# Optimization experiments

Measured on AMD Instinct MI355X. Metric: run time of the kernel, lower is better.

Reference implementation:

```python
import jax, jax.numpy as jnp
import numpy as np


def setup_inputs() -> dict:
    key = jax.random.key(0)
    ks = jax.random.split(key, 4)
    T, B, E = 2048, 2, 1024
    query = jax.random.normal(ks[0], (T, B, E), dtype=jnp.float32)
    attn_mask = jnp.zeros((T, T), dtype=jnp.float32)
    Wqkv = jax.random.normal(ks[1], (3 * E, E), dtype=jnp.float32) * 0.02
    bqkv = jnp.zeros((3 * E,), dtype=jnp.float32)
    Wout = jax.random.normal(ks[2], (E, E), dtype=jnp.float32) * 0.02
    bout = jnp.zeros((E,), dtype=jnp.float32)
    return {"query": query, "attn_mask": attn_mask, "Wqkv": Wqkv,
            "bqkv": bqkv, "Wout": Wout, "bout": bout, "num_heads": 16}


def reference(query, attn_mask, Wqkv, bqkv, Wout, bout, num_heads):
    T, B, E = query.shape
    H = num_heads
    hd = E // H
    scaling = hd ** -0.5
    # fused QKV projection: [T,B,3E]
    qkv = jnp.einsum('tbe,fe->tbf', query, Wqkv) + bqkv
    q, k, v = jnp.split(qkv, 3, axis=-1)
    q = q * scaling
    # [T,B,E] -> [B*H, T, hd]
    def to_heads(x):
        return x.reshape(T, B * H, hd).transpose(1, 0, 2)
    q, k, v = to_heads(q), to_heads(k), to_heads(v)
    # scores [B*H, T, T]
    scores = jnp.einsum('bth,bsh->bts', q, k) + attn_mask[None, :, :]
    probs = jax.nn.softmax(scores, axis=-1)  # dropout p=0
    attn = jnp.einsum('bts,bsh->bth', probs, v)  # [B*H, T, hd]
    attn = attn.transpose(1, 0, 2).reshape(T, B, E)
    out = jnp.einsum('tbe,fe->tbf', attn, Wout) + bout
    avg_w = probs.reshape(B, H, T, T).sum(axis=1) / H
    return out, avg_w
```

## Files before the change

kernel.cpp:

```cpp
#include <hip/hip_runtime.h>
#include <cstdint>
#include <cstddef>

#define Tt 2048
#define Bb 2
#define Ee 1024
#define Hh 16
#define HD 64
#define BHh (Bb*Hh)
#define Mm (Tt*Bb)

typedef short bf16x8 __attribute__((ext_vector_type(8)));
typedef float f32x4  __attribute__((ext_vector_type(4)));

#define MFMA16(a,b,c) __builtin_amdgcn_mfma_f32_16x16x32_bf16(a, b, c, 0, 0, 0)

__device__ __forceinline__ unsigned short f2bf(float f) {
    unsigned int u = __builtin_bit_cast(unsigned int, f);
    u += 0x7FFFu + ((u >> 16) & 1u);
    return (unsigned short)(u >> 16);
}
__device__ __forceinline__ unsigned int pack2bf(float lo, float hi) {
    return (unsigned int)f2bf(lo) | ((unsigned int)f2bf(hi) << 16);
}

__device__ __forceinline__ int swzA(int row, int dwcol) {
    return (row*32 + dwcol) ^ ((row & 7) << 2);
}
__device__ __forceinline__ int swzG(int row, int dwcol) {
    return (row*16 + dwcol) ^ ((row & 3) << 2);
}

__device__ __forceinline__ bf16x8 ldfrag(const unsigned short* base, int row, int col) {
    const unsigned int* p = (const unsigned int*)(base + row*66 + col);
    const unsigned int* q = (const unsigned int*)(base + row*66 + col + 16);
    uint4 u;
    u.x = p[0]; u.y = p[1];
    u.z = q[0]; u.w = q[1];
    return __builtin_bit_cast(bf16x8, u);
}

__global__ __launch_bounds__(256)
void to_bf16(const float* __restrict__ src, unsigned short* __restrict__ dst, int n8)
{
    const int stride = gridDim.x * 256;
    for (int i = blockIdx.x*256 + threadIdx.x; i < n8; i += stride) {
        const float4 a = ((const float4*)src)[2*i];
        const float4 b = ((const float4*)src)[2*i + 1];
        const uint4 u = {pack2bf(a.x,a.y), pack2bf(a.z,a.w),
                         pack2bf(b.x,b.y), pack2bf(b.z,b.w)};
        ((uint4*)dst)[i] = u;
    }
}

template<int MODE>
__global__ __launch_bounds__(256)
void gemm_mfma(const unsigned short* __restrict__ A, const unsigned short* __restrict__ W,
               const float* __restrict__ bias, float* __restrict__ Cout,
               unsigned short* __restrict__ qbuf, unsigned short* __restrict__ kbuf,
               unsigned short* __restrict__ vbuf, int N, int K)
{
    __shared__ __align__(16) unsigned int AsDW[2][128*16];
    __shared__ __align__(16) unsigned int WsDW[2][128*16];
    const int tid  = threadIdx.x;
    const int bm   = blockIdx.y * 128;
    const int bn   = blockIdx.x * 128;
    const int w    = tid >> 6;
    const int lane = tid & 63;
    const int lr   = lane & 15;
    const int lg   = lane >> 4;
    const int wm   = (w >> 1) * 64;
    const int wn   = (w & 1) * 64;

    f32x4 acc[4][4];
#pragma unroll
    for (int m = 0; m < 4; ++m)
#pragma unroll
        for (int n = 0; n < 4; ++n)
            acc[m][n] = f32x4{0.f, 0.f, 0.f, 0.f};

    const int r1  = tid >> 2;
    const int cdw = (tid & 3) * 4;

    {
        const uint4 a0 = *(const uint4*)&A[(size_t)(bm + r1)      * K + cdw*2];
        const uint4 a1 = *(const uint4*)&A[(size_t)(bm + r1 + 64) * K + cdw*2];
        const uint4 w0 = *(const uint4*)&W[(size_t)(bn + r1)      * K + cdw*2];
        const uint4 w1 = *(const uint4*)&W[(size_t)(bn + r1 + 64) * K + cdw*2];
        *(uint4*)(AsDW[0] + swzG(r1,      cdw)) = a0;
        *(uint4*)(AsDW[0] + swzG(r1 + 64, cdw)) = a1;
        *(uint4*)(WsDW[0] + swzG(r1,      cdw)) = w0;
        *(uint4*)(WsDW[0] + swzG(r1 + 64, cdw)) = w1;
        __syncthreads();
    }

    int cur = 0;
    for (int k0 = 0; k0 < K; k0 += 32) {
        const bool has_next = (k0 + 32 < K);
        uint4 an0, an1, wn0, wn1;
        if (has_next) {
            an0 = *(const uint4*)&A[(size_t)(bm + r1)      * K + k0 + 32 + cdw*2];
            an1 = *(const uint4*)&A[(size_t)(bm + r1 + 64) * K + k0 + 32 + cdw*2];
            wn0 = *(const uint4*)&W[(size_t)(bn + r1)      * K + k0 + 32 + cdw*2];
            wn1 = *(const uint4*)&W[(size_t)(bn + r1 + 64) * K + k0 + 32 + cdw*2];
        }

        const unsigned int* Ac = AsDW[cur];
        const unsigned int* Wc = WsDW[cur];
        bf16x8 af[4], wf[4];
#pragma unroll
        for (int i = 0; i < 4; ++i) {
            af[i] = __builtin_bit_cast(bf16x8, *(const uint4*)(Ac + swzG(wm + 16*i + lr, 4*lg)));
            wf[i] = __builtin_bit_cast(bf16x8, *(const uint4*)(Wc + swzG(wn + 16*i + lr, 4*lg)));
        }
#pragma unroll
        for (int m = 0; m < 4; ++m)
#pragma unroll
            for (int n = 0; n < 4; ++n)
                acc[m][n] = MFMA16(af[m], wf[n], acc[m][n]);

        if (has_next) {
            *(uint4*)(AsDW[cur ^ 1] + swzG(r1,      cdw)) = an0;
            *(uint4*)(AsDW[cur ^ 1] + swzG(r1 + 64, cdw)) = an1;
            *(uint4*)(WsDW[cur ^ 1] + swzG(r1,      cdw)) = wn0;
            *(uint4*)(WsDW[cur ^ 1] + swzG(r1 + 64, cdw)) = wn1;
        }
        __syncthreads();
        cur ^= 1;
    }

#pragma unroll
    for (int nsub = 0; nsub < 4; ++nsub) {
        const int n0 = bn + wn + 16*nsub + lr;
        const float bv = bias[n0];
#pragma unroll
        for (int msub = 0; msub < 4; ++msub) {
#pragma unroll
            for (int reg = 0; reg < 4; ++reg) {
                const int m = bm + wm + 16*msub + 4*lg + reg;
                float v = acc[msub][nsub][reg] + bv;
                if (MODE == 0) {
                    const int which = n0 >> 10;
                    const int e0 = n0 & 1023;
                    const int h = e0 >> 6, d0 = e0 & 63;
                    if (which == 0) v *= 0.125f;
                    unsigned short* dst = (which == 0) ? qbuf : (which == 1) ? kbuf : vbuf;
                    dst[((size_t)((m & 1)*Hh + h) * Tt + (m >> 1)) * HD + d0] = f2bf(v);
                } else {
                    Cout[(size_t)m * N + n0] = v;
                }
            }
        }
    }
}

__global__ __launch_bounds__(512)
void attn_mfma(const unsigned short* __restrict__ qb, const unsigned short* __restrict__ kb,
               const unsigned short* __restrict__ vb, const float* __restrict__ mask,
               unsigned short* __restrict__ attnb, float* __restrict__ lbuf)
{
    __shared__ __align__(16) unsigned int KsDW[2][64*32];
    __shared__ __align__(16) unsigned short Vt[2][64*66];
    __shared__ float l_sh[128];

    const int tid  = threadIdx.x;
    const int bid  = blockIdx.x;
    const int wid  = (bid & 7) * 64 + (bid >> 3);
    const int bh   = wid & 31;
    const int t0   = (wid >> 5) * 128;
    const int w    = tid >> 6;
    const int lane = tid & 63;
    const int lr   = lane & 15;
    const int lg   = lane >> 4;
    const int b = bh >> 4, h = bh & 15;

    const unsigned short* __restrict__ Qg = qb + (size_t)bh * Tt * HD;
    const unsigned short* __restrict__ Kg = kb + (size_t)bh * Tt * HD;
    const unsigned short* __restrict__ Vg = vb + (size_t)bh * Tt * HD;

    const int str = tid >> 3;
    const int sdw = (tid & 7) * 4;

    const int vdg = tid & 15;
    const int vs2 = tid >> 4;

    bf16x8 qf[2];
    for (int half = 0; half < 2; ++half) {
        __syncthreads();
        *(uint4*)(KsDW[0] + swzA(str, sdw)) =
            *(const uint4*)&Qg[(size_t)(t0 + half*64 + str) * HD + sdw*2];
        __syncthreads();
        if ((w >> 2) == half) {
            const int r = 16*(w & 3) + lr;
            qf[0] = __builtin_bit_cast(bf16x8, *(const uint4*)(KsDW[0] + swzA(r, 4*lg)));
            qf[1] = __builtin_bit_cast(bf16x8, *(const uint4*)(KsDW[0] + swzA(r, 16 + 4*lg)));
        }
    }

    f32x4 oacc[4];
#pragma unroll
    for (int d = 0; d < 4; ++d)
        oacc[d] = f32x4{0.f, 0.f, 0.f, 0.f};
    float lacc = 0.f;

    {
        const uint4 k0r = *(const uint4*)&Kg[(size_t)str * HD + sdw*2];
        const uint2 a0  = *(const uint2*)&Vg[(size_t)(2*vs2)     * HD + vdg*4];
        const uint2 c0  = *(const uint2*)&Vg[(size_t)(2*vs2 + 1) * HD + vdg*4];
        __syncthreads();
        *(uint4*)(KsDW[0] + swzA(str, sdw)) = k0r;
        unsigned short* vt0 = &Vt[0][0];
        *(unsigned int*)&vt0[(vdg*4+0)*66 + 2*vs2] = (a0.x & 0xFFFFu) | (c0.x << 16);
        *(unsigned int*)&vt0[(vdg*4+1)*66 + 2*vs2] = (a0.x >> 16)     | (c0.x & 0xFFFF0000u);
        *(unsigned int*)&vt0[(vdg*4+2)*66 + 2*vs2] = (a0.y & 0xFFFFu) | (c0.y << 16);
        *(unsigned int*)&vt0[(vdg*4+3)*66 + 2*vs2] = (a0.y >> 16)     | (c0.y & 0xFFFF0000u);
        __syncthreads();
    }

    int cur = 0;
    for (int s0 = 0; s0 < Tt; s0 += 64) {
        const bool has_next = (s0 + 64 < Tt);
        uint4 kn; uint2 van, vcn;
        if (has_next) {
            kn  = *(const uint4*)&Kg[(size_t)(s0 + 64 + str) * HD + sdw*2];
            van = *(const uint2*)&Vg[(size_t)(s0 + 64 + 2*vs2)     * HD + vdg*4];
            vcn = *(const uint2*)&Vg[(size_t)(s0 + 64 + 2*vs2 + 1) * HD + vdg*4];
        }

        const unsigned int* Kc = KsDW[cur];
        const unsigned short* Vc = &Vt[cur][0];

        f32x4 sacc[4];
#pragma unroll
        for (int ssub = 0; ssub < 4; ++ssub) {
            const bf16x8 a0 = __builtin_bit_cast(bf16x8,
                *(const uint4*)(Kc + swzA(16*ssub + lr, 4*lg)));
            const bf16x8 a1 = __builtin_bit_cast(bf16x8,
                *(const uint4*)(Kc + swzA(16*ssub + lr, 16 + 4*lg)));
            f32x4 z = {0.f, 0.f, 0.f, 0.f};
            z = MFMA16(a0, qf[0], z);
            z = MFMA16(a1, qf[1], z);
            sacc[ssub] = z;
        }

        unsigned int pw[8];
        {
            float lt = 0.f;
            const float* __restrict__ mrow =
                &mask[(size_t)(t0 + 16*w + lr) * Tt + s0];
#pragma unroll
            for (int ssub = 0; ssub < 4; ++ssub) {
                const float4 mv = *(const float4*)&mrow[16*ssub + 4*lg];
                const float e0 = __expf(sacc[ssub][0] + mv.x);
                const float e1 = __expf(sacc[ssub][1] + mv.y);
                const float e2 = __expf(sacc[ssub][2] + mv.z);
                const float e3 = __expf(sacc[ssub][3] + mv.w);
                lt += (e0 + e1) + (e2 + e3);
                pw[ssub*2]     = pack2bf(e0, e1);
                pw[ssub*2 + 1] = pack2bf(e2, e3);
            }
            lt += __shfl_xor(lt, 16);
            lt += __shfl_xor(lt, 32);
            lacc += lt;
        }

        const uint4 ua = {pw[0], pw[1], pw[2], pw[3]};
        const uint4 ub = {pw[4], pw[5], pw[6], pw[7]};
#pragma unroll
        for (int dsub = 0; dsub < 4; ++dsub) {
            const bf16x8 b0 = ldfrag(Vc, 16*dsub + lr, 4*lg);
            const bf16x8 b1 = ldfrag(Vc, 16*dsub + lr, 32 + 4*lg);
            oacc[dsub] = MFMA16(__builtin_bit_cast(bf16x8, ua), b0, oacc[dsub]);
            oacc[dsub] = MFMA16(__builtin_bit_cast(bf16x8, ub), b1, oacc[dsub]);
        }

        if (has_next) {
            *(uint4*)(KsDW[cur ^ 1] + swzA(str, sdw)) = kn;
            unsigned short* vt1 = &Vt[cur ^ 1][0];
            *(unsigned int*)&vt1[(vdg*4+0)*66 + 2*vs2] = (van.x & 0xFFFFu) | (vcn.x << 16);
            *(unsigned int*)&vt1[(vdg*4+1)*66 + 2*vs2] = (van.x >> 16)     | (vcn.x & 0xFFFF0000u);
            *(unsigned int*)&vt1[(vdg*4+2)*66 + 2*vs2] = (van.y & 0xFFFFu) | (vcn.y << 16);
            *(unsigned int*)&vt1[(vdg*4+3)*66 + 2*vs2] = (van.y >> 16)     | (vcn.y & 0xFFFF0000u);
        }
        __syncthreads();
        cur ^= 1;
    }

    if (lg == 0) l_sh[16*w + lr] = lacc;
    __syncthreads();
#pragma unroll
    for (int reg = 0; reg < 4; ++reg) {
        const int tl = 16*w + 4*lg + reg;
        const float inv = 1.f / l_sh[tl];
        const int t = t0 + tl;
#pragma unroll
        for (int dsub = 0; dsub < 4; ++dsub)
            attnb[((size_t)t * Bb + b) * Ee + h*HD + dsub*16 + lr] =
                f2bf(oacc[dsub][reg] * inv);
    }
    if (lg == 0)
        lbuf[(size_t)bh * Tt + t0 + 16*w + lr] = lacc;
}

__global__ __launch_bounds__(256)
void avg_probs_mfma(const unsigned short* __restrict__ qb, const unsigned short* __restrict__ kb,
                    const float* __restrict__ mask, const float* __restrict__ lbuf,
                    float* __restrict__ avg)
{
    __shared__ unsigned short Qs[64][66];
    __shared__ unsigned short Ksh[64][66];
    __shared__ float linv[16][64];

    const int tid  = threadIdx.x;
    const int b    = blockIdx.z;
    const int t0   = blockIdx.y * 64;
    const int s0   = blockIdx.x * 64;
    const int w    = tid >> 6;
    const int lane = tid & 63;
    const int lr   = lane & 15;
    const int lg   = lane >> 4;

    {
        const int h = tid >> 4, tl = (tid & 15) * 4;
        const float4 lv = *(const float4*)&lbuf[(size_t)(b*Hh + h) * Tt + t0 + tl];
        linv[h][tl+0] = 1.f / (16.f * lv.x);
        linv[h][tl+1] = 1.f / (16.f * lv.y);
        linv[h][tl+2] = 1.f / (16.f * lv.z);
        linv[h][tl+3] = 1.f / (16.f * lv.w);
    }

    f32x4 mf[4];
#pragma unroll
    for (int ssub = 0; ssub < 4; ++ssub)
#pragma unroll
        for (int reg = 0; reg < 4; ++reg)
            mf[ssub][reg] = mask[(size_t)(t0 + 16*w + 4*lg + reg) * Tt + s0 + 16*ssub + lr];

    f32x4 av[4];
#pragma unroll
    for (int ssub = 0; ssub < 4; ++ssub) av[ssub] = f32x4{0.f, 0.f, 0.f, 0.f};

    const int str = tid >> 2;
    const int stc = (tid & 3) * 16;

    for (int h = 0; h < Hh; ++h) {
        const unsigned short* __restrict__ Qg = qb + (size_t)(b*Hh + h) * Tt * HD;
        const unsigned short* __restrict__ Kg = kb + (size_t)(b*Hh + h) * Tt * HD;
        __syncthreads();
        {
            const unsigned short* Qp = &Qg[(size_t)(t0 + str) * HD + stc];
            const unsigned short* Kp = &Kg[(size_t)(s0 + str) * HD + stc];
            const uint4 q0 = *(const uint4*)Qp;
            const uint4 q1 = *(const uint4*)(Qp + 8);
            const uint4 k0 = *(const uint4*)Kp;
            const uint4 k1 = *(const uint4*)(Kp + 8);
            *(uint4*)&Qs[str][stc]      = q0;
            *(uint4*)&Qs[str][stc + 8]  = q1;
            *(uint4*)&Ksh[str][stc]     = k0;
            *(uint4*)&Ksh[str][stc + 8] = k1;
        }
        __syncthreads();

        const float lv0 = linv[h][16*w + 4*lg + 0];
        const float lv1 = linv[h][16*w + 4*lg + 1];
        const float lv2 = linv[h][16*w + 4*lg + 2];
        const float lv3 = linv[h][16*w + 4*lg + 3];

        const bf16x8 af0 = ldfrag(&Qs[0][0], 16*w + lr, 4*lg);
        const bf16x8 af1 = ldfrag(&Qs[0][0], 16*w + lr, 32 + 4*lg);
#pragma unroll
        for (int ssub = 0; ssub < 4; ++ssub) {
            const bf16x8 bf0 = ldfrag(&Ksh[0][0], 16*ssub + lr, 4*lg);
            const bf16x8 bf1 = ldfrag(&Ksh[0][0], 16*ssub + lr, 32 + 4*lg);
            f32x4 z = {0.f, 0.f, 0.f, 0.f};
            z = MFMA16(af0, bf0, z);
            z = MFMA16(af1, bf1, z);
            av[ssub][0] += __expf(z[0] + mf[ssub][0]) * lv0;
            av[ssub][1] += __expf(z[1] + mf[ssub][1]) * lv1;
            av[ssub][2] += __expf(z[2] + mf[ssub][2]) * lv2;
            av[ssub][3] += __expf(z[3] + mf[ssub][3]) * lv3;
        }
    }

#pragma unroll
    for (int ssub = 0; ssub < 4; ++ssub)
#pragma unroll
        for (int reg = 0; reg < 4; ++reg)
            avg[((size_t)b * Tt + t0 + 16*w + 4*lg + reg) * Tt + s0 + 16*ssub + lr] =
                av[ssub][reg];
}

extern "C" void kernel_launch(void* const* d_in, const int* in_sizes, int n_in,
                              void* d_out, int out_size, void* d_ws, size_t ws_size,
                              hipStream_t stream)
{
    (void)in_sizes; (void)n_in; (void)out_size; (void)ws_size;
    const float* query = (const float*)d_in[0];
    const float* mask  = (const float*)d_in[1];
    const float* Wqkv  = (const float*)d_in[2];
    const float* bqkv  = (const float*)d_in[3];
    const float* Wout  = (const float*)d_in[4];
    const float* bout  = (const float*)d_in[5];

    float* out = (float*)d_out;
    float* avg = out + (size_t)Tt * Bb * Ee;

    const size_t S1 = (size_t)BHh * Tt * HD;
    unsigned short* wsu     = (unsigned short*)d_ws;
    unsigned short* qbuf    = wsu;
    unsigned short* kbuf    = qbuf + S1;
    unsigned short* vbuf    = kbuf + S1;
    unsigned short* attnb   = vbuf + S1;
    unsigned short* querybf = attnb + (size_t)Mm * Ee;
    unsigned short* wqkvbf  = querybf + (size_t)Mm * Ee;
    unsigned short* woutbf  = wqkvbf + (size_t)3 * Ee * Ee;
    float*          lbuf    = (float*)(woutbf + (size_t)Ee * Ee);

    to_bf16<<<1024, 256, 0, stream>>>(query, querybf, (Mm*Ee)/8);
    to_bf16<<<1024, 256, 0, stream>>>(Wqkv, wqkvbf, (3*Ee*Ee)/8);
    to_bf16<<<512,  256, 0, stream>>>(Wout, woutbf, (Ee*Ee)/8);

    gemm_mfma<0><<<dim3(3072/128, Mm/128), 256, 0, stream>>>(
        querybf, wqkvbf, bqkv, nullptr, qbuf, kbuf, vbuf, 3072, Ee);
    attn_mfma<<<dim3(BHh * (Tt/128)), 512, 0, stream>>>(
        qbuf, kbuf, vbuf, mask, attnb, lbuf);
    avg_probs_mfma<<<dim3(Tt/64, Tt/64, Bb), 256, 0, stream>>>(
        qbuf, kbuf, mask, lbuf, avg);
    gemm_mfma<1><<<dim3(Ee/128, Mm/128), 256, 0, stream>>>(
        attnb, woutbf, bout, out, nullptr, nullptr, nullptr, Ee, Ee);
}
```

Measured before the change: 202.2 us.

## Process two query sub-tiles per wave in attention kernel to reuse K/V tiles

Each attention block now covers 256 query rows instead of 128, with every wave handling two 16-row query fragments. The K and V tiles loaded into LDS are reused across twice as many queries, which halves global K/V traffic and LDS staging per query. In exchange the grid shrinks to 256 blocks and per-thread register use grows (doubled accumulators and probabilities), which can lower occupancy and leave CUs underused on a large GPU.

```diff
diff --git a/kernel.cpp b/kernel.cpp
--- a/kernel.cpp
+++ b/kernel.cpp
@@ -161,13 +161,13 @@
 {
     __shared__ __align__(16) unsigned int KsDW[2][64*32];
     __shared__ __align__(16) unsigned short Vt[2][64*66];
-    __shared__ float l_sh[128];
+    __shared__ float l_sh[256];
 
     const int tid  = threadIdx.x;
     const int bid  = blockIdx.x;
-    const int wid  = (bid & 7) * 64 + (bid >> 3);
+    const int wid  = (bid & 7) * 32 + (bid >> 3);
     const int bh   = wid & 31;
-    const int t0   = (wid >> 5) * 128;
+    const int t0   = (wid >> 5) * 256;
     const int w    = tid >> 6;
     const int lane = tid & 63;
     const int lr   = lane & 15;
@@ -184,24 +184,29 @@
     const int vdg = tid & 15;
     const int vs2 = tid >> 4;
 
-    bf16x8 qf[2];
-    for (int half = 0; half < 2; ++half) {
+    bf16x8 qf[2][2];
+    for (int chunk = 0; chunk < 4; ++chunk) {
         __syncthreads();
         *(uint4*)(KsDW[0] + swzA(str, sdw)) =
-            *(const uint4*)&Qg[(size_t)(t0 + half*64 + str) * HD + sdw*2];
-        __syncthreads();
-        if ((w >> 2) == half) {
-            const int r = 16*(w & 3) + lr;
-            qf[0] = __builtin_bit_cast(bf16x8, *(const uint4*)(KsDW[0] + swzA(r, 4*lg)));
-            qf[1] = __builtin_bit_cast(bf16x8, *(const uint4*)(KsDW[0] + swzA(r, 16 + 4*lg)));
-        }
-    }
-
-    f32x4 oacc[4];
-#pragma unroll
-    for (int d = 0; d < 4; ++d)
-        oacc[d] = f32x4{0.f, 0.f, 0.f, 0.f};
-    float lacc = 0.f;
+            *(const uint4*)&Qg[(size_t)(t0 + chunk*64 + str) * HD + sdw*2];
+        __syncthreads();
+        if ((w >> 1) == chunk) {
+#pragma unroll
+            for (int u = 0; u < 2; ++u) {
+                const int r = 32*(w & 1) + 16*u + lr;
+                qf[u][0] = __builtin_bit_cast(bf16x8, *(const uint4*)(KsDW[0] + swzA(r, 4*lg)));
+                qf[u][1] = __builtin_bit_cast(bf16x8, *(const uint4*)(KsDW[0] + swzA(r, 16 + 4*lg)));
+            }
+        }
+    }
+
+    f32x4 oacc[2][4];
+#pragma unroll
+    for (int u = 0; u < 2; ++u)
+#pragma unroll
+        for (int d = 0; d < 4; ++d)
+            oacc[u][d] = f32x4{0.f, 0.f, 0.f, 0.f};
+    float lacc[2] = {0.f, 0.f};
 
     {
         const uint4 k0r = *(const uint4*)&Kg[(size_t)str * HD + sdw*2];
@@ -230,48 +235,55 @@
         const unsigned int* Kc = KsDW[cur];
         const unsigned short* Vc = &Vt[cur][0];
 
-        f32x4 sacc[4];
+        f32x4 sacc[2][4];
 #pragma unroll
         for (int ssub = 0; ssub < 4; ++ssub) {
             const bf16x8 a0 = __builtin_bit_cast(bf16x8,
                 *(const uint4*)(Kc + swzA(16*ssub + lr, 4*lg)));
             const bf16x8 a1 = __builtin_bit_cast(bf16x8,
                 *(const uint4*)(Kc + swzA(16*ssub + lr, 16 + 4*lg)));
-            f32x4 z = {0.f, 0.f, 0.f, 0.f};
-            z = MFMA16(a0, qf[0], z);
-            z = MFMA16(a1, qf[1], z);
-            sacc[ssub] = z;
-        }
-
-        unsigned int pw[8];
-        {
+#pragma unroll
+            for (int u = 0; u < 2; ++u) {
+                f32x4 z = {0.f, 0.f, 0.f, 0.f};
+                z = MFMA16(a0, qf[u][0], z);
+                z = MFMA16(a1, qf[u][1], z);
+                sacc[u][ssub] = z;
+            }
+        }
+
+        unsigned int pw[2][8];
+#pragma unroll
+        for (int u = 0; u < 2; ++u) {
             float lt = 0.f;
             const float* __restrict__ mrow =
-                &mask[(size_t)(t0 + 16*w + lr) * Tt + s0];
+                &mask[(size_t)(t0 + 32*w + 16*u + lr) * Tt + s0];
 #pragma unroll
             for (int ssub = 0; ssub < 4; ++ssub) {
                 const float4 mv = *(const float4*)&mrow[16*ssub + 4*lg];
-                const float e0 = __expf(sacc[ssub][0] + mv.x);
-                const float e1 = __expf(sacc[ssub][1] + mv.y);
-                const float e2 = __expf(sacc[ssub][2] + mv.z);
-                const float e3 = __expf(sacc[ssub][3] + mv.w);
+                const float e0 = __expf(sacc[u][ssub][0] + mv.x);
+                const float e1 = __expf(sacc[u][ssub][1] + mv.y);
+                const float e2 = __expf(sacc[u][ssub][2] + mv.z);
+                const float e3 = __expf(sacc[u][ssub][3] + mv.w);
                 lt += (e0 + e1) + (e2 + e3);
-                pw[ssub*2]     = pack2bf(e0, e1);
-                pw[ssub*2 + 1] = pack2bf(e2, e3);
+                pw[u][ssub*2]     = pack2bf(e0, e1);
+                pw[u][ssub*2 + 1] = pack2bf(e2, e3);
             }
             lt += __shfl_xor(lt, 16);
             lt += __shfl_xor(lt, 32);
-            lacc += lt;
-        }
-
-        const uint4 ua = {pw[0], pw[1], pw[2], pw[3]};
-        const uint4 ub = {pw[4], pw[5], pw[6], pw[7]};
+            lacc[u] += lt;
+        }
+
 #pragma unroll
         for (int dsub = 0; dsub < 4; ++dsub) {
             const bf16x8 b0 = ldfrag(Vc, 16*dsub + lr, 4*lg);
             const bf16x8 b1 = ldfrag(Vc, 16*dsub + lr, 32 + 4*lg);
-            oacc[dsub] = MFMA16(__builtin_bit_cast(bf16x8, ua), b0, oacc[dsub]);
-            oacc[dsub] = MFMA16(__builtin_bit_cast(bf16x8, ub), b1, oacc[dsub]);
+#pragma unroll
+            for (int u = 0; u < 2; ++u) {
+                const uint4 ua = {pw[u][0], pw[u][1], pw[u][2], pw[u][3]};
+                const uint4 ub = {pw[u][4], pw[u][5], pw[u][6], pw[u][7]};
+                oacc[u][dsub] = MFMA16(__builtin_bit_cast(bf16x8, ua), b0, oacc[u][dsub]);
+                oacc[u][dsub] = MFMA16(__builtin_bit_cast(bf16x8, ub), b1, oacc[u][dsub]);
+            }
         }
 
         if (has_next) {
@@ -286,20 +298,26 @@
         cur ^= 1;
     }
 
-    if (lg == 0) l_sh[16*w + lr] = lacc;
+    if (lg == 0) {
+        l_sh[32*w + lr]      = lacc[0];
+        l_sh[32*w + 16 + lr] = lacc[1];
+    }
     __syncthreads();
 #pragma unroll
-    for (int reg = 0; reg < 4; ++reg) {
-        const int tl = 16*w + 4*lg + reg;
-        const float inv = 1.f / l_sh[tl];
-        const int t = t0 + tl;
-#pragma unroll
-        for (int dsub = 0; dsub < 4; ++dsub)
-            attnb[((size_t)t * Bb + b) * Ee + h*HD + dsub*16 + lr] =
-                f2bf(oacc[dsub][reg] * inv);
-    }
-    if (lg == 0)
-        lbuf[(size_t)bh * Tt + t0 + 16*w + lr] = lacc;
+    for (int u = 0; u < 2; ++u) {
+#pragma unroll
+        for (int reg = 0; reg < 4; ++reg) {
+            const int tl = 32*w + 16*u + 4*lg + reg;
+            const float inv = 1.f / l_sh[tl];
+            const int t = t0 + tl;
+#pragma unroll
+            for (int dsub = 0; dsub < 4; ++dsub)
+                attnb[((size_t)t * Bb + b) * Ee + h*HD + dsub*16 + lr] =
+                    f2bf(oacc[u][dsub][reg] * inv);
+        }
+        if (lg == 0)
+            lbuf[(size_t)bh * Tt + t0 + 32*w + 16*u + lr] = lacc[u];
+    }
 }
 
 __global__ __launch_bounds__(256)
@@ -422,7 +440,7 @@
 
     gemm_mfma<0><<<dim3(3072/128, Mm/128), 256, 0, stream>>>(
         querybf, wqkvbf, bqkv, nullptr, qbuf, kbuf, vbuf, 3072, Ee);
-    attn_mfma<<<dim3(BHh * (Tt/128)), 512, 0, stream>>>(
+    attn_mfma<<<dim3(BHh * (Tt/256)), 512, 0, stream>>>(
         qbuf, kbuf, vbuf, mask, attnb, lbuf);
     avg_probs_mfma<<<dim3(Tt/64, Tt/64, Bb), 256, 0, stream>>>(
         qbuf, kbuf, mask, lbuf, avg);
```

Result: slower. 238.7 us (+18.0%).
